# Optimization experiments

Hardware: AMD Instinct MI355X
Metric: run time of the kernel (lower is better)

The kernel has to match this reference:

```python
import jax, jax.numpy as jnp
import numpy as np

N_EL = 4            # allowed elements (H, C, N, O)
N_EXPERTS = N_EL * N_EL
F_ATOM = 176        # per-atom symmetry feature dim
F_PAIR = 32         # pair feature dim (2*F_ATOM + F_PAIR == 384 == nodes[0])


def _init_linear(key, fin, fout, n):
    # torch nn.Linear default init: U(-1/sqrt(fin), 1/sqrt(fin))
    bound = 1.0 / np.sqrt(fin)
    kw, kb = jax.random.split(key)
    W = jax.random.uniform(kw, (n, fin, fout), minval=-bound, maxval=bound, dtype=jnp.float32)
    b = jax.random.uniform(kb, (n, fout), minval=-bound, maxval=bound, dtype=jnp.float32)
    return W, b


def setup_inputs() -> dict:
    key = jax.random.key(0)
    ks = jax.random.split(key, 8)
    B, A, C = 128, 128, 256
    elements = jax.random.randint(ks[0], (B, A), 0, N_EL)
    connectivity = jax.random.randint(ks[1], (B, C, 2), 0, A)
    sym_features = jax.random.normal(ks[2], (B, A, F_ATOM), dtype=jnp.float32)
    pair_features = jax.random.normal(ks[3], (B, C, F_PAIR), dtype=jnp.float32)
    W1, b1 = _init_linear(ks[4], 384, 128, N_EXPERTS)
    W2, b2 = _init_linear(ks[5], 128, 96, N_EXPERTS)
    W3, b3 = _init_linear(ks[6], 96, 2, N_EXPERTS)
    return dict(elements=elements, connectivity=connectivity,
                sym_features=sym_features, pair_features=pair_features,
                W1=W1, b1=b1, W2=W2, b2=b2, W3=W3, b3=b3)


def _pair_moe(elements, connectivity, sym_features, pair_features, W1, b1, W2, b2, W3, b3):
    B, C, _ = connectivity.shape
    A = sym_features.shape[1]
    out_dim = W3.shape[-1]

    # mirror: mask padded pairs (connectivity[...,0] == -1) before offsetting
    mask = (connectivity[..., 0] != -1).reshape(-1)              # [B*C]
    conn_f = (connectivity + (jnp.arange(B) * A)[:, None, None]).reshape(-1, 2)
    idx0 = jnp.where(mask, conn_f[:, 0], 0)
    idx1 = jnp.where(mask, conn_f[:, 1], 0)

    feat_f = sym_features.reshape(-1, sym_features.shape[-1])    # [B*A, F]
    el_f = elements.reshape(-1)                                  # [B*A]

    m = mask[:, None].astype(sym_features.dtype)
    fa = feat_f[idx0] * m                                        # [B*C, F] (zeros where padded)
    fb = feat_f[idx1] * m
    e0 = jnp.where(mask, el_f[idx0], -1)
    e1 = jnp.where(mask, el_f[idx1], -1)
    nn_index = e0 * N_EL + e1                                    # -5 for padded pairs -> no expert

    x = jnp.concatenate([fa, fb, pair_features.reshape(-1, pair_features.shape[-1])], axis=1)

    y = jnp.zeros((x.shape[0], out_dim), dtype=x.dtype)
    for i in range(N_EXPERTS):  # fixed small expert set (structural loop)
        h = jax.nn.celu(x @ W1[i] + b1[i])
        h = jax.nn.celu(h @ W2[i] + b2[i])
        o = h @ W3[i] + b3[i]
        y = jnp.where((nn_index == i)[:, None], o, y)
    return y.reshape(B, C, out_dim)


def reference(elements, connectivity, sym_features, pair_features, W1, b1, W2, b2, W3, b3):
    # Original returns (elements, connectivity, y); only y is computed output.
    return _pair_moe(elements, connectivity, sym_features, pair_features, W1, b1, W2, b2, W3, b3)
```

## Files before the change

kernel.cpp:

```cpp
#include <hip/hip_runtime.h>
#include <math.h>

typedef __attribute__((ext_vector_type(8))) short short8;
typedef __attribute__((ext_vector_type(4))) float f32x4;

namespace {
constexpr int NEL   = 4;
constexpr int NEXP  = 16;
constexpr int Bb    = 128;
constexpr int Aa    = 128;
constexpr int Cc    = 256;
constexpr int FATOM = 176;
constexpr int FPAIR = 32;
constexpr int FIN   = 384;
constexpr int HH1   = 128;
constexpr int HH2   = 96;
constexpr int NP    = Bb * Cc;
constexpr int NA    = Bb * Aa;
constexpr int BUCKET_CAP = 4096;

constexpr int WS_COUNTS = 0;
constexpr int WS_B2     = 64;
constexpr int WS_SHORTS = 64 + NEXP * BUCKET_CAP * 4;

constexpr int W2_OFF = 12 * HH1 * 32;
constexpr int WPK_E  = W2_OFF + 4 * HH2 * 32;
constexpr int WPK_N  = NEXP * WPK_E;

constexpr int SYM_N  = NA * FATOM;
constexpr int PAIR_N = NP * FPAIR;

constexpr int CVT_BLOCKS = (SYM_N / 4 + PAIR_N / 4) / 256;
constexpr int W1_BLOCKS  = 768;
constexpr int W2_BLOCKS  = 192;
constexpr int IDX_BLOCKS = NP / 256;
constexpr int W1_BASE  = CVT_BLOCKS;
constexpr int W2_BASE  = W1_BASE + W1_BLOCKS;
constexpr int IDX_BASE = W2_BASE + W2_BLOCKS;
constexpr int PREP_GRID = IDX_BASE + IDX_BLOCKS;
}

__device__ inline short f2bf(float f) {
    unsigned u = __builtin_bit_cast(unsigned, f);
    unsigned r = (u + 0x7FFFu + ((u >> 16) & 1u)) >> 16;
    return (short)r;
}
__device__ inline float celu1(float v) {
    return v > 0.f ? v : (__expf(v) - 1.0f);
}
__device__ inline void gl_lds16(const short* g, short* l) {
    __builtin_amdgcn_global_load_lds(
        (const __attribute__((address_space(1))) void*)g,
        (__attribute__((address_space(3))) void*)l, 16, 0, 0);
}

__global__ __launch_bounds__(256) void k_prep(
    const float* __restrict__ sym, const float* __restrict__ pairf,
    short* __restrict__ symb, short* __restrict__ pairfb,
    const float* __restrict__ W1, const float* __restrict__ W2,
    short* __restrict__ wpk,
    const int* __restrict__ conn, const int* __restrict__ elements,
    int* __restrict__ counts, int4* __restrict__ bucket2,
    float* __restrict__ out)
{
    __shared__ float T[32][33];
    __shared__ int sh_cnt[NEXP], sh_base[NEXP];

    int bid = blockIdx.x;
    int t = threadIdx.x;

    if (bid < CVT_BLOCKS) {
        int i = bid * 256 + t;
        constexpr int NS4 = SYM_N / 4;
        const float4* src; short* dst; int j;
        if (i < NS4) { src = (const float4*)sym;   dst = symb;   j = i; }
        else         { src = (const float4*)pairf; dst = pairfb; j = i - NS4; }
        float4 v = src[j];
        short4 o;
        o.x = f2bf(v.x); o.y = f2bf(v.y); o.z = f2bf(v.z); o.w = f2bf(v.w);
        *(short4*)(dst + 4 * (size_t)j) = o;
    } else if (bid < IDX_BASE) {
        const float* src; short* dst; int N, k0, n0;
        if (bid < W2_BASE) {
            int b1i = bid - W1_BASE;
            int e = b1i / 48, tl = b1i % 48;
            N = HH1; k0 = (tl % 12) * 32; n0 = (tl / 12) * 32;
            src = W1 + (size_t)e * FIN * HH1;
            dst = wpk + (size_t)e * WPK_E;
        } else {
            int b2i = bid - W2_BASE;
            int e = b2i / 12, tl = b2i % 12;
            N = HH2; k0 = (tl % 4) * 32; n0 = (tl / 4) * 32;
            src = W2 + (size_t)e * HH1 * HH2;
            dst = wpk + (size_t)e * WPK_E + W2_OFF;
        }
        int tx = t & 31, ty = t >> 5;
        int ks = k0 >> 5;
#pragma unroll
        for (int j = 0; j < 4; ++j) {
            int r = ty + 8 * j;
            T[r][tx] = src[(size_t)(k0 + r) * N + n0 + tx];
        }
        __syncthreads();
#pragma unroll
        for (int j = 0; j < 4; ++j) {
            int n = n0 + ty + 8 * j;
            dst[(size_t)(ks * N + n) * 32 + tx] = f2bf(T[tx][ty + 8 * j]);
        }
    } else {
        int p = (bid - IDX_BASE) * 256 + t;
        if (t < NEXP) sh_cnt[t] = 0;
        __syncthreads();
        int e = -1, r = 0, i0 = 0, i1 = 0;
        {
            int c0 = conn[2 * p], c1 = conn[2 * p + 1];
            if (c0 != -1) {
                int b = p / Cc;
                i0 = b * Aa + c0; if (i0 < 0) i0 += NA;
                i1 = b * Aa + c1; if (i1 < 0) i1 += NA;
                e = elements[i0] * NEL + elements[i1];
            }
            if (e < 0 || e >= NEXP) {
                out[2 * p] = 0.f; out[2 * p + 1] = 0.f;
                e = -1;
            } else {
                r = atomicAdd(&sh_cnt[e], 1);
            }
        }
        __syncthreads();
        if (t < NEXP) sh_base[t] = (sh_cnt[t] > 0) ? atomicAdd(&counts[t], sh_cnt[t]) : 0;
        __syncthreads();
        if (e >= 0) {
            int pos = sh_base[e] + r;
            if (pos < BUCKET_CAP) {
                int4 rec; rec.x = p; rec.y = i0; rec.z = i1; rec.w = 0;
                bucket2[e * BUCKET_CAP + pos] = rec;
            }
        }
    }
}

#define GATHER2(A, REC) do {                                                  \
    const short* fa = symb + (size_t)((REC).y & (NA - 1)) * FATOM;            \
    const short* fb = symb + (size_t)((REC).z & (NA - 1)) * FATOM;            \
    const short* pf = pairfb + (size_t)((REC).x & (NP - 1)) * FPAIR;          \
    A[0]  = *(const short8*)(fa + 8 * lg);                                    \
    A[1]  = *(const short8*)(fa + 32 + 8 * lg);                               \
    A[2]  = *(const short8*)(fa + 64 + 8 * lg);                               \
    A[3]  = *(const short8*)(fa + 96 + 8 * lg);                               \
    A[4]  = *(const short8*)(fa + 128 + 8 * lg);                              \
    A[5]  = *(const short8*)((lg < 2 ? fa + 160 : fb - 16) + 8 * lg);         \
    A[6]  = *(const short8*)(fb + 16 + 8 * lg);                               \
    A[7]  = *(const short8*)(fb + 48 + 8 * lg);                               \
    A[8]  = *(const short8*)(fb + 80 + 8 * lg);                               \
    A[9]  = *(const short8*)(fb + 112 + 8 * lg);                              \
    A[10] = *(const short8*)(fb + 144 + 8 * lg);                              \
    A[11] = *(const short8*)(pf + 8 * lg);                                    \
} while (0)

__global__ void __launch_bounds__(512)
__attribute__((amdgpu_waves_per_eu(2, 2)))
k_moe(
    const int* __restrict__ counts, const int4* __restrict__ bucket2,
    const short* __restrict__ symb, const short* __restrict__ pairfb,
    const short* __restrict__ wpk,
    const float* __restrict__ b1, const float* __restrict__ b2,
    const float* __restrict__ W3, const float* __restrict__ b3,
    float* __restrict__ out)
{
    __shared__ __align__(16) short Wlds[WPK_E];
    __shared__ __align__(16) short H1s[8][16 * HH1];

    int e     = blockIdx.x & 15;
    int shard = blockIdx.x >> 4;
    int cnt = counts[e];
    if (cnt > BUCKET_CAP) cnt = BUCKET_CAP;
    int nt = (cnt + 31) >> 5;

    int t = threadIdx.x;
    int w = t >> 6;
    int lane = t & 63;
    int lr = lane & 15, lg = (lane >> 4) & 3;

    const int4* b2e = bucket2 + e * BUCKET_CAP;
    const short* wsrc = wpk + (size_t)e * WPK_E;

    int tile = w * 16 + shard;
    bool active = tile < nt;

    int ii0 = tile * 32 + lr;
    int ii1 = ii0 + 16;
    int cm1 = cnt > 0 ? cnt - 1 : 0;
    int4 rec0 = b2e[active ? (ii0 < cnt ? ii0 : cm1) : 0];
    int4 rec1 = b2e[active ? (ii1 < cnt ? ii1 : cm1) : 0];
    short8 aA[12], aB[12];
    GATHER2(aA, rec0);
    GATHER2(aB, rec1);
    __builtin_amdgcn_sched_barrier(0);

#pragma unroll
    for (int r = 0; r < 15; ++r)
        gl_lds16(wsrc + r * 4096 + t * 8, &Wlds[r * 4096 + t * 8]);
    float b1v[8];
#pragma unroll
    for (int j = 0; j < 8; ++j) b1v[j] = b1[e * HH1 + j * 16 + lr];
    float2 b3v = ((const float2*)b3)[e];

    __syncthreads();
    if (!active) return;

    short* h1w = &H1s[w][0];

    f32x4 acc[2][8];
#pragma unroll
    for (int j = 0; j < 8; ++j) {
        acc[0][j] = (f32x4){b1v[j], b1v[j], b1v[j], b1v[j]};
        acc[1][j] = acc[0][j];
    }
#pragma unroll
    for (int ks = 0; ks < 12; ++ks) {
#pragma unroll
        for (int j = 0; j < 8; ++j) {
            short8 bw = *(const short8*)&Wlds[(ks * HH1 + j * 16 + lr) * 32 + 8 * lg];
            acc[0][j] = __builtin_amdgcn_mfma_f32_16x16x32_bf16(aA[ks], bw, acc[0][j], 0, 0, 0);
            acc[1][j] = __builtin_amdgcn_mfma_f32_16x16x32_bf16(aB[ks], bw, acc[1][j], 0, 0, 0);
        }
    }

#pragma unroll
    for (int mi = 0; mi < 2; ++mi) {
#pragma unroll
        for (int j = 0; j < 8; ++j)
#pragma unroll
            for (int r2 = 0; r2 < 4; ++r2) {
                int m = 4 * lg + r2;
                int n = 16 * j + lr;
                h1w[m * HH1 + (((n >> 3) ^ (m & 7)) << 3) + (n & 7)] = f2bf(celu1(acc[mi][j][r2]));
            }
        asm volatile("s_waitcnt lgkmcnt(0)" ::: "memory");
        __builtin_amdgcn_sched_barrier(0);

        int mx = lr & 7;
        short8 bh0 = *(const short8*)&h1w[lr * HH1 + (((0 + lg) ^ mx) << 3)];
        short8 bh1 = *(const short8*)&h1w[lr * HH1 + (((4 + lg) ^ mx) << 3)];
        short8 bh2 = *(const short8*)&h1w[lr * HH1 + (((8 + lg) ^ mx) << 3)];
        short8 bh3 = *(const short8*)&h1w[lr * HH1 + (((12 + lg) ^ mx) << 3)];

        float s0 = 0.f, s1 = 0.f;
#pragma unroll
        for (int t6 = 0; t6 < 6; ++t6) {
            int n2b = 16 * t6 + 4 * lg;
            float4 bb4 = *(const float4*)&b2[e * HH2 + n2b];
            f32x4 a2c;
            a2c[0] = bb4.x; a2c[1] = bb4.y; a2c[2] = bb4.z; a2c[3] = bb4.w;
            {
                short8 aw = *(const short8*)&Wlds[W2_OFF + (0 * HH2 + 16 * t6 + lr) * 32 + 8 * lg];
                a2c = __builtin_amdgcn_mfma_f32_16x16x32_bf16(aw, bh0, a2c, 0, 0, 0);
            }
            {
                short8 aw = *(const short8*)&Wlds[W2_OFF + (1 * HH2 + 16 * t6 + lr) * 32 + 8 * lg];
                a2c = __builtin_amdgcn_mfma_f32_16x16x32_bf16(aw, bh1, a2c, 0, 0, 0);
            }
            {
                short8 aw = *(const short8*)&Wlds[W2_OFF + (2 * HH2 + 16 * t6 + lr) * 32 + 8 * lg];
                a2c = __builtin_amdgcn_mfma_f32_16x16x32_bf16(aw, bh2, a2c, 0, 0, 0);
            }
            {
                short8 aw = *(const short8*)&Wlds[W2_OFF + (3 * HH2 + 16 * t6 + lr) * 32 + 8 * lg];
                a2c = __builtin_amdgcn_mfma_f32_16x16x32_bf16(aw, bh3, a2c, 0, 0, 0);
            }
            float4 w3a = *(const float4*)&W3[(size_t)(e * HH2 + n2b) * 2];
            float4 w3b = *(const float4*)&W3[(size_t)(e * HH2 + n2b) * 2 + 4];
            float h0 = celu1(a2c[0]), h1c = celu1(a2c[1]), h2 = celu1(a2c[2]), h3 = celu1(a2c[3]);
            s0 = fmaf(h0, w3a.x, fmaf(h1c, w3a.z, fmaf(h2, w3b.x, fmaf(h3, w3b.z, s0))));
            s1 = fmaf(h0, w3a.y, fmaf(h1c, w3a.w, fmaf(h2, w3b.y, fmaf(h3, w3b.w, s1))));
        }
        s0 += __shfl_xor(s0, 16); s0 += __shfl_xor(s0, 32);
        s1 += __shfl_xor(s1, 16); s1 += __shfl_xor(s1, 32);
        int ii = mi == 0 ? ii0 : ii1;
        int pp = (mi == 0 ? rec0.x : rec1.x) & (NP - 1);
        if (((lane >> 4) & 3) == 0 && ii < cnt) {
            float2 o2; o2.x = s0 + b3v.x; o2.y = s1 + b3v.y;
            *(float2*)(out + 2 * (size_t)pp) = o2;
        }
    }
}

extern "C" void kernel_launch(void* const* d_in, const int* in_sizes, int n_in,
                              void* d_out, int out_size, void* d_ws, size_t ws_size,
                              hipStream_t stream)
{
    const int*   elements = (const int*)d_in[0];
    const int*   conn     = (const int*)d_in[1];
    const float* sym      = (const float*)d_in[2];
    const float* pairf    = (const float*)d_in[3];
    const float* W1       = (const float*)d_in[4];
    const float* b1       = (const float*)d_in[5];
    const float* W2       = (const float*)d_in[6];
    const float* b2       = (const float*)d_in[7];
    const float* W3       = (const float*)d_in[8];
    const float* b3       = (const float*)d_in[9];
    float* out = (float*)d_out;

    int* wsi     = (int*)d_ws;
    int* counts  = wsi + WS_COUNTS;
    int4* bucket2 = (int4*)(wsi + WS_B2);

    short* sbase  = (short*)(wsi + WS_SHORTS);
    short* wpk    = sbase;
    short* symb   = sbase + WPK_N;
    short* pairfb = sbase + WPK_N + SYM_N;

    hipMemsetAsync((void*)counts, 0, NEXP * sizeof(int), stream);

    k_prep<<<PREP_GRID, 256, 0, stream>>>(sym, pairf, symb, pairfb,
                                          W1, W2, wpk,
                                          conn, elements, counts, bucket2, out);
    k_moe<<<256, 512, 0, stream>>>(counts, bucket2, symb, pairfb, wpk,
                                   b1, b2, W3, b3, out);
}
```

Baseline: 32.38 us.

## Fuse bf16 conversion into gather and use four waves looping over tiles

Removes the separate prep pass that converted all atom and pair features to bf16. The MoE kernel now gathers fp32 rows directly and converts them in registers. Only four of the eight waves compute; each handles two 16-row sub-tiles at once, using two LDS H1 buffers so the layer-2 MFMAs for both can interleave, and loops over further tiles. This saves a full read and write of the feature arrays but doubles gather bytes, halves active waves per block, and serialises tiles within a wave.

```diff
diff --git a/kernel.cpp b/kernel.cpp
--- a/kernel.cpp
+++ b/kernel.cpp
@@ -27,16 +27,11 @@
 constexpr int WPK_E  = W2_OFF + 4 * HH2 * 32;
 constexpr int WPK_N  = NEXP * WPK_E;
 
-constexpr int SYM_N  = NA * FATOM;
-constexpr int PAIR_N = NP * FPAIR;
-
-constexpr int CVT_BLOCKS = (SYM_N / 4 + PAIR_N / 4) / 256;
 constexpr int W1_BLOCKS  = 768;
 constexpr int W2_BLOCKS  = 192;
 constexpr int IDX_BLOCKS = NP / 256;
-constexpr int W1_BASE  = CVT_BLOCKS;
-constexpr int W2_BASE  = W1_BASE + W1_BLOCKS;
-constexpr int IDX_BASE = W2_BASE + W2_BLOCKS;
+constexpr int W2_BASE  = W1_BLOCKS;
+constexpr int IDX_BASE = W1_BLOCKS + W2_BLOCKS;
 constexpr int PREP_GRID = IDX_BASE + IDX_BLOCKS;
 }
 
@@ -48,6 +43,14 @@
 __device__ inline float celu1(float v) {
     return v > 0.f ? v : (__expf(v) - 1.0f);
 }
+__device__ inline short8 cvt8(const float* p) {
+    float4 lo = *(const float4*)p;
+    float4 hi = *(const float4*)(p + 4);
+    short8 r;
+    r[0] = f2bf(lo.x); r[1] = f2bf(lo.y); r[2] = f2bf(lo.z); r[3] = f2bf(lo.w);
+    r[4] = f2bf(hi.x); r[5] = f2bf(hi.y); r[6] = f2bf(hi.z); r[7] = f2bf(hi.w);
+    return r;
+}
 __device__ inline void gl_lds16(const short* g, short* l) {
     __builtin_amdgcn_global_load_lds(
         (const __attribute__((address_space(1))) void*)g,
@@ -55,8 +58,6 @@
 }
 
 __global__ __launch_bounds__(256) void k_prep(
-    const float* __restrict__ sym, const float* __restrict__ pairf,
-    short* __restrict__ symb, short* __restrict__ pairfb,
     const float* __restrict__ W1, const float* __restrict__ W2,
     short* __restrict__ wpk,
     const int* __restrict__ conn, const int* __restrict__ elements,
@@ -69,21 +70,10 @@
     int bid = blockIdx.x;
     int t = threadIdx.x;
 
-    if (bid < CVT_BLOCKS) {
-        int i = bid * 256 + t;
-        constexpr int NS4 = SYM_N / 4;
-        const float4* src; short* dst; int j;
-        if (i < NS4) { src = (const float4*)sym;   dst = symb;   j = i; }
-        else         { src = (const float4*)pairf; dst = pairfb; j = i - NS4; }
-        float4 v = src[j];
-        short4 o;
-        o.x = f2bf(v.x); o.y = f2bf(v.y); o.z = f2bf(v.z); o.w = f2bf(v.w);
-        *(short4*)(dst + 4 * (size_t)j) = o;
-    } else if (bid < IDX_BASE) {
+    if (bid < IDX_BASE) {
         const float* src; short* dst; int N, k0, n0;
         if (bid < W2_BASE) {
-            int b1i = bid - W1_BASE;
-            int e = b1i / 48, tl = b1i % 48;
+            int e = bid / 48, tl = bid % 48;
             N = HH1; k0 = (tl % 12) * 32; n0 = (tl / 12) * 32;
             src = W1 + (size_t)e * FIN * HH1;
             dst = wpk + (size_t)e * WPK_E;
@@ -140,29 +130,29 @@
     }
 }
 
-#define GATHER2(A, REC) do {                                                  \
-    const short* fa = symb + (size_t)((REC).y & (NA - 1)) * FATOM;            \
-    const short* fb = symb + (size_t)((REC).z & (NA - 1)) * FATOM;            \
-    const short* pf = pairfb + (size_t)((REC).x & (NP - 1)) * FPAIR;          \
-    A[0]  = *(const short8*)(fa + 8 * lg);                                    \
-    A[1]  = *(const short8*)(fa + 32 + 8 * lg);                               \
-    A[2]  = *(const short8*)(fa + 64 + 8 * lg);                               \
-    A[3]  = *(const short8*)(fa + 96 + 8 * lg);                               \
-    A[4]  = *(const short8*)(fa + 128 + 8 * lg);                              \
-    A[5]  = *(const short8*)((lg < 2 ? fa + 160 : fb - 16) + 8 * lg);         \
-    A[6]  = *(const short8*)(fb + 16 + 8 * lg);                               \
-    A[7]  = *(const short8*)(fb + 48 + 8 * lg);                               \
-    A[8]  = *(const short8*)(fb + 80 + 8 * lg);                               \
-    A[9]  = *(const short8*)(fb + 112 + 8 * lg);                              \
-    A[10] = *(const short8*)(fb + 144 + 8 * lg);                              \
-    A[11] = *(const short8*)(pf + 8 * lg);                                    \
+#define GATHERF(A, REC) do {                                                  \
+    const float* fa = sym + (size_t)((REC).y & (NA - 1)) * FATOM;             \
+    const float* fb = sym + (size_t)((REC).z & (NA - 1)) * FATOM;             \
+    const float* pf = pairf + (size_t)((REC).x & (NP - 1)) * FPAIR;           \
+    A[0]  = cvt8(fa + 8 * lg);                                                \
+    A[1]  = cvt8(fa + 32 + 8 * lg);                                           \
+    A[2]  = cvt8(fa + 64 + 8 * lg);                                           \
+    A[3]  = cvt8(fa + 96 + 8 * lg);                                           \
+    A[4]  = cvt8(fa + 128 + 8 * lg);                                          \
+    A[5]  = cvt8((lg < 2 ? fa + 160 : fb - 16) + 8 * lg);                     \
+    A[6]  = cvt8(fb + 16 + 8 * lg);                                           \
+    A[7]  = cvt8(fb + 48 + 8 * lg);                                           \
+    A[8]  = cvt8(fb + 80 + 8 * lg);                                           \
+    A[9]  = cvt8(fb + 112 + 8 * lg);                                          \
+    A[10] = cvt8(fb + 144 + 8 * lg);                                          \
+    A[11] = cvt8(pf + 8 * lg);                                                \
 } while (0)
 
 __global__ void __launch_bounds__(512)
 __attribute__((amdgpu_waves_per_eu(2, 2)))
 k_moe(
     const int* __restrict__ counts, const int4* __restrict__ bucket2,
-    const short* __restrict__ symb, const short* __restrict__ pairfb,
+    const float* __restrict__ sym, const float* __restrict__ pairf,
     const short* __restrict__ wpk,
     const float* __restrict__ b1, const float* __restrict__ b2,
     const float* __restrict__ W3, const float* __restrict__ b3,
@@ -186,16 +176,17 @@
     const short* wsrc = wpk + (size_t)e * WPK_E;
 
     int tile = w * 16 + shard;
-    bool active = tile < nt;
+    bool wactive = (w < 4);
+    bool active = wactive && tile < nt;
+    int cm1 = cnt > 0 ? cnt - 1 : 0;
 
     int ii0 = tile * 32 + lr;
     int ii1 = ii0 + 16;
-    int cm1 = cnt > 0 ? cnt - 1 : 0;
     int4 rec0 = b2e[active ? (ii0 < cnt ? ii0 : cm1) : 0];
     int4 rec1 = b2e[active ? (ii1 < cnt ? ii1 : cm1) : 0];
     short8 aA[12], aB[12];
-    GATHER2(aA, rec0);
-    GATHER2(aB, rec1);
+    GATHERF(aA, rec0);
+    GATHERF(aB, rec1);
     __builtin_amdgcn_sched_barrier(0);
 
 #pragma unroll
@@ -207,82 +198,113 @@
     float2 b3v = ((const float2*)b3)[e];
 
     __syncthreads();
-    if (!active) return;
-
-    short* h1w = &H1s[w][0];
-
-    f32x4 acc[2][8];
-#pragma unroll
-    for (int j = 0; j < 8; ++j) {
-        acc[0][j] = (f32x4){b1v[j], b1v[j], b1v[j], b1v[j]};
-        acc[1][j] = acc[0][j];
-    }
-#pragma unroll
-    for (int ks = 0; ks < 12; ++ks) {
-#pragma unroll
-        for (int j = 0; j < 8; ++j) {
-            short8 bw = *(const short8*)&Wlds[(ks * HH1 + j * 16 + lr) * 32 + 8 * lg];
-            acc[0][j] = __builtin_amdgcn_mfma_f32_16x16x32_bf16(aA[ks], bw, acc[0][j], 0, 0, 0);
-            acc[1][j] = __builtin_amdgcn_mfma_f32_16x16x32_bf16(aB[ks], bw, acc[1][j], 0, 0, 0);
-        }
-    }
-
-#pragma unroll
-    for (int mi = 0; mi < 2; ++mi) {
-#pragma unroll
-        for (int j = 0; j < 8; ++j)
-#pragma unroll
-            for (int r2 = 0; r2 < 4; ++r2) {
-                int m = 4 * lg + r2;
-                int n = 16 * j + lr;
-                h1w[m * HH1 + (((n >> 3) ^ (m & 7)) << 3) + (n & 7)] = f2bf(celu1(acc[mi][j][r2]));
-            }
-        asm volatile("s_waitcnt lgkmcnt(0)" ::: "memory");
-        __builtin_amdgcn_sched_barrier(0);
-
-        int mx = lr & 7;
-        short8 bh0 = *(const short8*)&h1w[lr * HH1 + (((0 + lg) ^ mx) << 3)];
-        short8 bh1 = *(const short8*)&h1w[lr * HH1 + (((4 + lg) ^ mx) << 3)];
-        short8 bh2 = *(const short8*)&h1w[lr * HH1 + (((8 + lg) ^ mx) << 3)];
-        short8 bh3 = *(const short8*)&h1w[lr * HH1 + (((12 + lg) ^ mx) << 3)];
-
-        float s0 = 0.f, s1 = 0.f;
-#pragma unroll
-        for (int t6 = 0; t6 < 6; ++t6) {
-            int n2b = 16 * t6 + 4 * lg;
-            float4 bb4 = *(const float4*)&b2[e * HH2 + n2b];
-            f32x4 a2c;
-            a2c[0] = bb4.x; a2c[1] = bb4.y; a2c[2] = bb4.z; a2c[3] = bb4.w;
-            {
-                short8 aw = *(const short8*)&Wlds[W2_OFF + (0 * HH2 + 16 * t6 + lr) * 32 + 8 * lg];
-                a2c = __builtin_amdgcn_mfma_f32_16x16x32_bf16(aw, bh0, a2c, 0, 0, 0);
-            }
-            {
-                short8 aw = *(const short8*)&Wlds[W2_OFF + (1 * HH2 + 16 * t6 + lr) * 32 + 8 * lg];
-                a2c = __builtin_amdgcn_mfma_f32_16x16x32_bf16(aw, bh1, a2c, 0, 0, 0);
-            }
-            {
-                short8 aw = *(const short8*)&Wlds[W2_OFF + (2 * HH2 + 16 * t6 + lr) * 32 + 8 * lg];
-                a2c = __builtin_amdgcn_mfma_f32_16x16x32_bf16(aw, bh2, a2c, 0, 0, 0);
-            }
-            {
-                short8 aw = *(const short8*)&Wlds[W2_OFF + (3 * HH2 + 16 * t6 + lr) * 32 + 8 * lg];
-                a2c = __builtin_amdgcn_mfma_f32_16x16x32_bf16(aw, bh3, a2c, 0, 0, 0);
-            }
-            float4 w3a = *(const float4*)&W3[(size_t)(e * HH2 + n2b) * 2];
-            float4 w3b = *(const float4*)&W3[(size_t)(e * HH2 + n2b) * 2 + 4];
-            float h0 = celu1(a2c[0]), h1c = celu1(a2c[1]), h2 = celu1(a2c[2]), h3 = celu1(a2c[3]);
-            s0 = fmaf(h0, w3a.x, fmaf(h1c, w3a.z, fmaf(h2, w3b.x, fmaf(h3, w3b.z, s0))));
-            s1 = fmaf(h0, w3a.y, fmaf(h1c, w3a.w, fmaf(h2, w3b.y, fmaf(h3, w3b.w, s1))));
-        }
-        s0 += __shfl_xor(s0, 16); s0 += __shfl_xor(s0, 32);
-        s1 += __shfl_xor(s1, 16); s1 += __shfl_xor(s1, 32);
-        int ii = mi == 0 ? ii0 : ii1;
-        int pp = (mi == 0 ? rec0.x : rec1.x) & (NP - 1);
-        if (((lane >> 4) & 3) == 0 && ii < cnt) {
-            float2 o2; o2.x = s0 + b3v.x; o2.y = s1 + b3v.y;
-            *(float2*)(out + 2 * (size_t)pp) = o2;
-        }
+    if (!wactive) return;
+
+    short* h1A = &H1s[w][0];
+    short* h1B = &H1s[w + 4][0];
+
+    for (;;) {
+        if (tile < nt) {
+            f32x4 acc[2][8];
+#pragma unroll
+            for (int j = 0; j < 8; ++j) {
+                acc[0][j] = (f32x4){b1v[j], b1v[j], b1v[j], b1v[j]};
+                acc[1][j] = acc[0][j];
+            }
+#pragma unroll
+            for (int ks = 0; ks < 12; ++ks) {
+#pragma unroll
+                for (int j = 0; j < 8; ++j) {
+                    short8 bw = *(const short8*)&Wlds[(ks * HH1 + j * 16 + lr) * 32 + 8 * lg];
+                    acc[0][j] = __builtin_amdgcn_mfma_f32_16x16x32_bf16(aA[ks], bw, acc[0][j], 0, 0, 0);
+                    acc[1][j] = __builtin_amdgcn_mfma_f32_16x16x32_bf16(aB[ks], bw, acc[1][j], 0, 0, 0);
+                }
+            }
+
+#pragma unroll
+            for (int j = 0; j < 8; ++j)
+#pragma unroll
+                for (int r2 = 0; r2 < 4; ++r2) {
+                    int m = 4 * lg + r2;
+                    int n = 16 * j + lr;
+                    int off = m * HH1 + (((n >> 3) ^ (m & 7)) << 3) + (n & 7);
+                    h1A[off] = f2bf(celu1(acc[0][j][r2]));
+                    h1B[off] = f2bf(celu1(acc[1][j][r2]));
+                }
+            asm volatile("s_waitcnt lgkmcnt(0)" ::: "memory");
+            __builtin_amdgcn_sched_barrier(0);
+
+            int mx = lr & 7;
+            short8 bhA0 = *(const short8*)&h1A[lr * HH1 + (((0 + lg) ^ mx) << 3)];
+            short8 bhA1 = *(const short8*)&h1A[lr * HH1 + (((4 + lg) ^ mx) << 3)];
+            short8 bhA2 = *(const short8*)&h1A[lr * HH1 + (((8 + lg) ^ mx) << 3)];
+            short8 bhA3 = *(const short8*)&h1A[lr * HH1 + (((12 + lg) ^ mx) << 3)];
+            short8 bhB0 = *(const short8*)&h1B[lr * HH1 + (((0 + lg) ^ mx) << 3)];
+            short8 bhB1 = *(const short8*)&h1B[lr * HH1 + (((4 + lg) ^ mx) << 3)];
+            short8 bhB2 = *(const short8*)&h1B[lr * HH1 + (((8 + lg) ^ mx) << 3)];
+            short8 bhB3 = *(const short8*)&h1B[lr * HH1 + (((12 + lg) ^ mx) << 3)];
+
+            float sA0 = 0.f, sA1 = 0.f, sB0 = 0.f, sB1 = 0.f;
+#pragma unroll
+            for (int t6 = 0; t6 < 6; ++t6) {
+                int n2b = 16 * t6 + 4 * lg;
+                float4 bb4 = *(const float4*)&b2[e * HH2 + n2b];
+                f32x4 ac0, ac1;
+                ac0[0] = bb4.x; ac0[1] = bb4.y; ac0[2] = bb4.z; ac0[3] = bb4.w;
+                ac1 = ac0;
+                {
+                    short8 aw = *(const short8*)&Wlds[W2_OFF + (0 * HH2 + 16 * t6 + lr) * 32 + 8 * lg];
+                    ac0 = __builtin_amdgcn_mfma_f32_16x16x32_bf16(aw, bhA0, ac0, 0, 0, 0);
+                    ac1 = __builtin_amdgcn_mfma_f32_16x16x32_bf16(aw, bhB0, ac1, 0, 0, 0);
+                }
+                {
+                    short8 aw = *(const short8*)&Wlds[W2_OFF + (1 * HH2 + 16 * t6 + lr) * 32 + 8 * lg];
+                    ac0 = __builtin_amdgcn_mfma_f32_16x16x32_bf16(aw, bhA1, ac0, 0, 0, 0);
+                    ac1 = __builtin_amdgcn_mfma_f32_16x16x32_bf16(aw, bhB1, ac1, 0, 0, 0);
+                }
+                {
+                    short8 aw = *(const short8*)&Wlds[W2_OFF + (2 * HH2 + 16 * t6 + lr) * 32 + 8 * lg];
+                    ac0 = __builtin_amdgcn_mfma_f32_16x16x32_bf16(aw, bhA2, ac0, 0, 0, 0);
+                    ac1 = __builtin_amdgcn_mfma_f32_16x16x32_bf16(aw, bhB2, ac1, 0, 0, 0);
+                }
+                {
+                    short8 aw = *(const short8*)&Wlds[W2_OFF + (3 * HH2 + 16 * t6 + lr) * 32 + 8 * lg];
+                    ac0 = __builtin_amdgcn_mfma_f32_16x16x32_bf16(aw, bhA3, ac0, 0, 0, 0);
+                    ac1 = __builtin_amdgcn_mfma_f32_16x16x32_bf16(aw, bhB3, ac1, 0, 0, 0);
+                }
+                float4 w3a = *(const float4*)&W3[(size_t)(e * HH2 + n2b) * 2];
+                float4 w3b = *(const float4*)&W3[(size_t)(e * HH2 + n2b) * 2 + 4];
+                float hA0 = celu1(ac0[0]), hA1 = celu1(ac0[1]), hA2 = celu1(ac0[2]), hA3 = celu1(ac0[3]);
+                float hB0 = celu1(ac1[0]), hB1 = celu1(ac1[1]), hB2 = celu1(ac1[2]), hB3 = celu1(ac1[3]);
+                sA0 = fmaf(hA0, w3a.x, fmaf(hA1, w3a.z, fmaf(hA2, w3b.x, fmaf(hA3, w3b.z, sA0))));
+                sA1 = fmaf(hA0, w3a.y, fmaf(hA1, w3a.w, fmaf(hA2, w3b.y, fmaf(hA3, w3b.w, sA1))));
+                sB0 = fmaf(hB0, w3a.x, fmaf(hB1, w3a.z, fmaf(hB2, w3b.x, fmaf(hB3, w3b.z, sB0))));
+                sB1 = fmaf(hB0, w3a.y, fmaf(hB1, w3a.w, fmaf(hB2, w3b.y, fmaf(hB3, w3b.w, sB1))));
+            }
+            sA0 += __shfl_xor(sA0, 16); sA0 += __shfl_xor(sA0, 32);
+            sA1 += __shfl_xor(sA1, 16); sA1 += __shfl_xor(sA1, 32);
+            sB0 += __shfl_xor(sB0, 16); sB0 += __shfl_xor(sB0, 32);
+            sB1 += __shfl_xor(sB1, 16); sB1 += __shfl_xor(sB1, 32);
+            if (((lane >> 4) & 3) == 0) {
+                if (ii0 < cnt) {
+                    float2 o2; o2.x = sA0 + b3v.x; o2.y = sA1 + b3v.y;
+                    *(float2*)(out + 2 * (size_t)(rec0.x & (NP - 1))) = o2;
+                }
+                if (ii1 < cnt) {
+                    float2 o2; o2.x = sB0 + b3v.x; o2.y = sB1 + b3v.y;
+                    *(float2*)(out + 2 * (size_t)(rec1.x & (NP - 1))) = o2;
+                }
+            }
+        }
+
+        tile += 64;
+        if (tile >= nt) break;
+        ii0 = tile * 32 + lr;
+        ii1 = ii0 + 16;
+        rec0 = b2e[ii0 < cnt ? ii0 : cm1];
+        rec1 = b2e[ii1 < cnt ? ii1 : cm1];
+        GATHERF(aA, rec0);
+        GATHERF(aB, rec1);
     }
 }
 
@@ -305,17 +327,12 @@
     int* wsi     = (int*)d_ws;
     int* counts  = wsi + WS_COUNTS;
     int4* bucket2 = (int4*)(wsi + WS_B2);
-
-    short* sbase  = (short*)(wsi + WS_SHORTS);
-    short* wpk    = sbase;
-    short* symb   = sbase + WPK_N;
-    short* pairfb = sbase + WPK_N + SYM_N;
+    short* wpk   = (short*)(wsi + WS_SHORTS);
 
     hipMemsetAsync((void*)counts, 0, NEXP * sizeof(int), stream);
 
-    k_prep<<<PREP_GRID, 256, 0, stream>>>(sym, pairf, symb, pairfb,
-                                          W1, W2, wpk,
-                                          conn, elements, counts, bucket2, out);
-    k_moe<<<256, 512, 0, stream>>>(counts, bucket2, symb, pairfb, wpk,
+    k_prep<<<PREP_GRID, 256, 0, stream>>>(W1, W2, wpk, conn, elements,
+                                          counts, bucket2, out);
+    k_moe<<<256, 512, 0, stream>>>(counts, bucket2, sym, pairf, wpk,
                                    b1, b2, W3, b3, out);
 }
```

Result: slower. 62.99 us (+94.5%).
